# Performance work log

Measured on AMD Instinct MI355X. Metric: run time of the kernel, lower is better.

The kernel has to match this reference:

```python
import jax, jax.numpy as jnp
import numpy as np

EMBED_DIM = 1024
NUM_HEADS = 16
HEAD_DIM = EMBED_DIM // NUM_HEADS  # 64
SCALE = HEAD_DIM ** -0.5


def _rope_table(seq_len, dtype=jnp.float32):
    # inv_freq: [head_dim/2]
    inv_freq = 1.0 / (10000.0 ** (jnp.arange(0, HEAD_DIM, 2, dtype=dtype) / HEAD_DIM))
    t = jnp.arange(seq_len, dtype=dtype)
    freqs = t[:, None] * inv_freq[None, :]  # [S, hd/2]
    return jnp.sin(freqs), jnp.cos(freqs)


def _apply_rope(x, sin, cos):
    # x: [B, H, S, hd]; sin/cos: [S, hd/2]
    sin = sin[None, None]
    cos = cos[None, None]
    x_even = x[..., 0::2]
    x_odd = x[..., 1::2]
    new_even = x_even * cos - x_odd * sin
    new_odd = x_even * sin + x_odd * cos
    # interleave back: [..., hd/2, 2] -> [..., hd]
    return jnp.stack((new_even, new_odd), axis=-1).reshape(x.shape)


def setup_inputs() -> dict:
    key = jax.random.key(0)
    ks = jax.random.split(key, 9)
    B, S, D = 2, 2048, EMBED_DIM
    s = D ** -0.5
    return {
        "query": jax.random.normal(ks[0], (B, S, D), dtype=jnp.float32),
        "Wq": jax.random.normal(ks[1], (2 * D, D), dtype=jnp.float32) * s,
        "bq": jnp.zeros((2 * D,), dtype=jnp.float32),
        "Wk": jax.random.normal(ks[2], (D, D), dtype=jnp.float32) * s,
        "bk": jnp.zeros((D,), dtype=jnp.float32),
        "Wv": jax.random.normal(ks[3], (D, D), dtype=jnp.float32) * s,
        "bv": jnp.zeros((D,), dtype=jnp.float32),
        "Wo": jax.random.normal(ks[4], (D, D), dtype=jnp.float32) * s,
        "bo": jnp.zeros((D,), dtype=jnp.float32),
    }


def reference(query, Wq, bq, Wk, bk, Wv, bv, Wo, bo):
    B, S, D = query.shape
    H, hd = NUM_HEADS, HEAD_DIM

    # QKV projections (elementwise-gate variant: q_proj outputs 2*D)
    q_raw = (query @ Wq.T + bq).reshape(B, S, H, 2 * hd)
    q = q_raw[..., :hd].transpose(0, 2, 1, 3)          # [B,H,S,hd]
    gate = q_raw[..., hd:].transpose(0, 2, 1, 3)        # [B,H,S,hd]
    k = (query @ Wk.T + bk).reshape(B, S, H, hd).transpose(0, 2, 1, 3)
    v = (query @ Wv.T + bv).reshape(B, S, H, hd).transpose(0, 2, 1, 3)

    sin, cos = _rope_table(S)
    q = _apply_rope(q, sin, cos)
    k = _apply_rope(k, sin, cos)

    # scaled dot-product attention (no mask, non-causal, dropout=0)
    scores = jnp.einsum('bhqd,bhkd->bhqk', q, k) * SCALE
    probs = jax.nn.softmax(scores, axis=-1)
    attn = jnp.einsum('bhqk,bhkd->bhqd', probs, v)

    # sigmoid elementwise gate, then output projection
    attn = attn * jax.nn.sigmoid(gate)
    out = attn.transpose(0, 2, 1, 3).reshape(B, S, D)
    return out @ Wo.T + bo
```

## Files before the change

kernel.cpp:

```cpp
#include <hip/hip_runtime.h>
#include <math.h>

#define SEQ 2048
#define DIMD 1024
#define NH 16
#define HDIM 64

typedef _Float16 h8 __attribute__((ext_vector_type(8)));
typedef _Float16 h4 __attribute__((ext_vector_type(4)));
typedef __fp16 fp16x2 __attribute__((ext_vector_type(2)));
typedef float f32x4 __attribute__((ext_vector_type(4)));

typedef const __attribute__((address_space(1))) void* gas_t;
typedef __attribute__((address_space(3))) void* las_t;

__device__ __forceinline__ int SWE(int r, int c) {
  return ((r << 6) + c) ^ ((r & 7) << 3);
}

#define R0 16384
#define R1 (R0 + 1048576)
#define R2 (R1 + 524288)
#define R3 (R2 + 262144)
#define R4 (R3 + 262144)
#define R5 (R4 + 262144)

__global__ void prep_kernel(const float* __restrict__ query,
                            const float* __restrict__ Wq,
                            const float* __restrict__ Wk,
                            const float* __restrict__ Wv,
                            const float* __restrict__ Wo,
                            _Float16* __restrict__ Ah,
                            _Float16* __restrict__ Wqh,
                            _Float16* __restrict__ Wkh,
                            _Float16* __restrict__ Wvh,
                            _Float16* __restrict__ Woh,
                            float* __restrict__ sintab,
                            float* __restrict__ costab) {
  int i = blockIdx.x * 256 + threadIdx.x;
  if (i < R0) {
#pragma unroll
    for (int j = 0; j < 4; ++j) {
      int idx = i * 4 + j;
      int tp = idx >> 5;
      int fi = idx & 31;
      double inv = pow(10000.0, -(double)(2 * fi) / 64.0);
      double a = (double)tp * inv;
      sintab[idx] = (float)sin(a);
      costab[idx] = (float)cos(a);
    }
    return;
  }
  const float* src;
  _Float16* dst;
  int k;
  if (i < R1) {
    k = i - R0; src = query; dst = Ah;
  } else if (i < R2) {
    k = i - R1; src = Wq; dst = Wqh;
  } else if (i < R3) {
    k = i - R2; src = Wk; dst = Wkh;
  } else if (i < R4) {
    k = i - R3; src = Wv; dst = Wvh;
  } else if (i < R5) {
    k = i - R4; src = Wo; dst = Woh;
  } else {
    return;
  }
  float4 v = ((const float4*)src)[k];
  h4 H;
  H[0] = (_Float16)v.x;
  H[1] = (_Float16)v.y;
  H[2] = (_Float16)v.z;
  H[3] = (_Float16)v.w;
  ((h4*)dst)[k] = H;
}

__global__ __launch_bounds__(256) void qkv_kernel(
    const _Float16* __restrict__ Ah, const _Float16* __restrict__ Wqh,
    const _Float16* __restrict__ Wkh, const _Float16* __restrict__ Wvh,
    const float* __restrict__ bq, const float* __restrict__ bk,
    const float* __restrict__ bv, _Float16* __restrict__ qw,
    _Float16* __restrict__ sg, _Float16* __restrict__ kw,
    _Float16* __restrict__ vtw, const float* __restrict__ sintab,
    const float* __restrict__ costab) {
  __shared__ _Float16 Abuf[8192];
  __shared__ _Float16 Bbuf[8192];
  const int t = threadIdx.x;
  const int lane = t & 63;
  const int w = t >> 6;
  const int wm = w & 1, wn = w >> 1;
  const int fr = lane & 15;
  const int g = lane >> 4;
  const int m0 = blockIdx.y * 128;
  const int n0 = blockIdx.x * 128;
  const int region = (n0 < 2048) ? 0 : (n0 < 3072 ? 1 : 2);
  const _Float16* Wb = region == 0   ? Wqh + (size_t)n0 * DIMD
                       : region == 1 ? Wkh + (size_t)(n0 - 2048) * DIMD
                                     : Wvh + (size_t)(n0 - 3072) * DIMD;
  const float* bias = region == 0   ? bq + n0
                      : region == 1 ? bk + (n0 - 2048)
                                    : bv + (n0 - 3072);

  f32x4 acc[4][4];
#pragma unroll
  for (int i = 0; i < 4; ++i)
#pragma unroll
    for (int j = 0; j < 4; ++j) acc[i][j] = (f32x4){0.f, 0.f, 0.f, 0.f};

  const int rsub = t >> 3;
  const int csw = ((t & 7) ^ (rsub & 7)) << 3;
  const _Float16* gA = Ah + (size_t)(m0 + rsub) * DIMD + csw;
  const _Float16* gB = Wb + (size_t)rsub * DIMD + csw;
  const int dbase = (t >> 6) * 512 + 0;

  for (int kt = 0; kt < 16; ++kt) {
#pragma unroll
    for (int i = 0; i < 4; ++i) {
      __builtin_amdgcn_global_load_lds(
          (gas_t)(gA + (size_t)i * 32 * DIMD + kt * 64),
          (las_t)&Abuf[i * 2048 + w * 512], 16, 0, 0);
      __builtin_amdgcn_global_load_lds(
          (gas_t)(gB + (size_t)i * 32 * DIMD + kt * 64),
          (las_t)&Bbuf[i * 2048 + w * 512], 16, 0, 0);
    }
    __syncthreads();
#pragma unroll
    for (int s = 0; s < 2; ++s) {
      h8 av[4], bv[4];
#pragma unroll
      for (int mi = 0; mi < 4; ++mi)
        av[mi] = *(const h8*)&Abuf[SWE(wm * 64 + mi * 16 + fr, 8 * g + 32 * s)];
#pragma unroll
      for (int ni = 0; ni < 4; ++ni)
        bv[ni] = *(const h8*)&Bbuf[SWE(wn * 64 + ni * 16 + fr, 8 * g + 32 * s)];
      __builtin_amdgcn_s_setprio(1);
#pragma unroll
      for (int mi = 0; mi < 4; ++mi)
#pragma unroll
        for (int ni = 0; ni < 4; ++ni)
          acc[mi][ni] = __builtin_amdgcn_mfma_f32_16x16x32_f16(
              av[mi], bv[ni], acc[mi][ni], 0, 0, 0);
      __builtin_amdgcn_s_setprio(0);
    }
    __syncthreads();
  }

#pragma unroll
  for (int mi = 0; mi < 4; ++mi)
#pragma unroll
    for (int ni = 0; ni < 4; ++ni) {
      const int cl = wn * 64 + ni * 16 + fr;
      const float bsv = bias[cl];
      if (region == 2) {
        const int vc = (n0 - 3072) + cl;
        const int h = vc >> 6, d = vc & 63;
        const int row0 = m0 + wm * 64 + mi * 16 + g * 4;
        const int b = row0 >> 11;
        const int s0 = row0 & (SEQ - 1);
        h4 vv;
#pragma unroll
        for (int r = 0; r < 4; ++r) vv[r] = (_Float16)(acc[mi][ni][r] + bsv);
        *(h4*)&vtw[((size_t)(b * NH + h) * HDIM + d) * SEQ + s0] = vv;
        continue;
      }
#pragma unroll
      for (int r = 0; r < 4; ++r) {
        const int row = m0 + wm * 64 + mi * 16 + g * 4 + r;
        float v = acc[mi][ni][r] + bsv;
        const int b = row >> 11;
        const int s = row & (SEQ - 1);
        if (region == 0) {
          const int h = n0 >> 7;
          const int d = cl & 63;
          if (wn == 0) {
            float vp = __shfl_xor(v, 1);
            const int pi = s * 32 + (d >> 1);
            float sn = sintab[pi], cs = costab[pi];
            float rv = (d & 1) ? (vp * sn + v * cs) : (v * cs - vp * sn);
            rv *= 0.125f;
            qw[((size_t)(b * NH + h) * SEQ + s) * HDIM + d] = (_Float16)rv;
          } else {
            float gv = 1.0f / (1.0f + __expf(-v));
            sg[((size_t)(b * SEQ + s)) * DIMD + h * HDIM + d] = (_Float16)gv;
          }
        } else {
          const int kc = (n0 - 2048) + cl;
          const int h = kc >> 6, d = kc & 63;
          float vp = __shfl_xor(v, 1);
          const int pi = s * 32 + (d >> 1);
          float sn = sintab[pi], cs = costab[pi];
          float rv = (d & 1) ? (vp * sn + v * cs) : (v * cs - vp * sn);
          kw[((size_t)(b * NH + h) * SEQ + s) * HDIM + d] = (_Float16)rv;
        }
      }
    }
}

__global__ __launch_bounds__(256) void ogemm_kernel(
    const _Float16* __restrict__ ag, const _Float16* __restrict__ Woh,
    const float* __restrict__ bias, float* __restrict__ out) {
  __shared__ _Float16 Abuf[8192];
  __shared__ _Float16 Bbuf[4096];
  const int t = threadIdx.x;
  const int lane = t & 63;
  const int w = t >> 6;
  const int wm = w & 1, wn = w >> 1;
  const int fr = lane & 15;
  const int g = lane >> 4;
  const int m0 = blockIdx.y * 128, n0 = blockIdx.x * 64;

  f32x4 acc[4][2];
#pragma unroll
  for (int i = 0; i < 4; ++i)
#pragma unroll
    for (int j = 0; j < 2; ++j) acc[i][j] = (f32x4){0.f, 0.f, 0.f, 0.f};

  const int rsub = t >> 3;
  const int csw = ((t & 7) ^ (rsub & 7)) << 3;
  const _Float16* gA = ag + (size_t)(m0 + rsub) * DIMD + csw;
  const _Float16* gB = Woh + (size_t)(n0 + rsub) * DIMD + csw;

  for (int kt = 0; kt < 16; ++kt) {
#pragma unroll
    for (int i = 0; i < 4; ++i)
      __builtin_amdgcn_global_load_lds(
          (gas_t)(gA + (size_t)i * 32 * DIMD + kt * 64),
          (las_t)&Abuf[i * 2048 + w * 512], 16, 0, 0);
#pragma unroll
    for (int i = 0; i < 2; ++i)
      __builtin_amdgcn_global_load_lds(
          (gas_t)(gB + (size_t)i * 32 * DIMD + kt * 64),
          (las_t)&Bbuf[i * 2048 + w * 512], 16, 0, 0);
    __syncthreads();
#pragma unroll
    for (int s = 0; s < 2; ++s) {
      h8 av[4], bv[2];
#pragma unroll
      for (int mi = 0; mi < 4; ++mi)
        av[mi] = *(const h8*)&Abuf[SWE(wm * 64 + mi * 16 + fr, 8 * g + 32 * s)];
#pragma unroll
      for (int ni = 0; ni < 2; ++ni)
        bv[ni] = *(const h8*)&Bbuf[SWE(wn * 32 + ni * 16 + fr, 8 * g + 32 * s)];
      __builtin_amdgcn_s_setprio(1);
#pragma unroll
      for (int mi = 0; mi < 4; ++mi)
#pragma unroll
        for (int ni = 0; ni < 2; ++ni)
          acc[mi][ni] = __builtin_amdgcn_mfma_f32_16x16x32_f16(
              av[mi], bv[ni], acc[mi][ni], 0, 0, 0);
      __builtin_amdgcn_s_setprio(0);
    }
    __syncthreads();
  }

#pragma unroll
  for (int mi = 0; mi < 4; ++mi)
#pragma unroll
    for (int ni = 0; ni < 2; ++ni) {
      const int col = n0 + wn * 32 + ni * 16 + fr;
      const float bsv = bias[col];
#pragma unroll
      for (int r = 0; r < 4; ++r) {
        const int row = m0 + wm * 64 + mi * 16 + g * 4 + r;
        out[(size_t)row * DIMD + col] = acc[mi][ni][r] + bsv;
      }
    }
}

__global__ __launch_bounds__(256) void flash_kernel(
    const _Float16* __restrict__ qh, const _Float16* __restrict__ kh,
    const _Float16* __restrict__ vt, const _Float16* __restrict__ sg,
    _Float16* __restrict__ ag) {
  __shared__ _Float16 K_lds[4096];
  __shared__ _Float16 Vt_lds[4096];
  const int t = threadIdx.x;
  const int lane = t & 63;
  const int w = t >> 6;
  const int fr = lane & 15;
  const int g = lane >> 4;
  const int flat = blockIdx.x;
  const int swz = (flat & 7) * 128 + (flat >> 3);
  const int bh = swz >> 5;
  const int q0 = (swz & 31) * 64;
  const size_t kvbase = (size_t)bh * (SEQ * HDIM);

  h8 qb[2];
  {
    const _Float16* qp = qh + kvbase + (size_t)(q0 + 16 * w + fr) * HDIM + 8 * g;
    qb[0] = *(const h8*)(qp);
    qb[1] = *(const h8*)(qp + 32);
  }

  f32x4 oacc[4];
  float m_i = -1e30f, l_i = 0.f;
#pragma unroll
  for (int df = 0; df < 4; ++df) oacc[df] = (f32x4){0.f, 0.f, 0.f, 0.f};

  const int srow = t >> 2;
  const int scb = (t & 3) * 16;
  const _Float16* kp = kh + kvbase;
  const _Float16* vp = vt + kvbase + (size_t)srow * SEQ;

  h8 k0v = *(const h8*)(kp + (size_t)srow * HDIM + scb);
  h8 k1v = *(const h8*)(kp + (size_t)srow * HDIM + scb + 8);
  h8 v0v = *(const h8*)(vp + scb);
  h8 v1v = *(const h8*)(vp + scb + 8);

  for (int j0 = 0; j0 < SEQ; j0 += 64) {
    __syncthreads();
    *(h8*)&K_lds[SWE(srow, scb)] = k0v;
    *(h8*)&K_lds[SWE(srow, scb + 8)] = k1v;
    *(h8*)&Vt_lds[SWE(srow, scb)] = v0v;
    *(h8*)&Vt_lds[SWE(srow, scb + 8)] = v1v;
    if (j0 + 64 < SEQ) {
      k0v = *(const h8*)(kp + (size_t)(j0 + 64 + srow) * HDIM + scb);
      k1v = *(const h8*)(kp + (size_t)(j0 + 64 + srow) * HDIM + scb + 8);
      v0v = *(const h8*)(vp + j0 + 64 + scb);
      v1v = *(const h8*)(vp + j0 + 64 + scb + 8);
    }
    __syncthreads();

    f32x4 sacc[4];
#pragma unroll
    for (int nf = 0; nf < 4; ++nf) sacc[nf] = (f32x4){0.f, 0.f, 0.f, 0.f};

    __builtin_amdgcn_s_setprio(1);
#pragma unroll
    for (int nf = 0; nf < 4; ++nf) {
      h8 ka0 = *(const h8*)&K_lds[SWE(16 * nf + fr, 8 * g)];
      h8 ka1 = *(const h8*)&K_lds[SWE(16 * nf + fr, 32 + 8 * g)];
      sacc[nf] =
          __builtin_amdgcn_mfma_f32_16x16x32_f16(ka0, qb[0], sacc[nf], 0, 0, 0);
      sacc[nf] =
          __builtin_amdgcn_mfma_f32_16x16x32_f16(ka1, qb[1], sacc[nf], 0, 0, 0);
    }
    __builtin_amdgcn_s_setprio(0);

    float m0 = fmaxf(fmaxf(sacc[0][0], sacc[0][1]), sacc[0][2]);
    float m1 = fmaxf(fmaxf(sacc[0][3], sacc[1][0]), sacc[1][1]);
    float m2 = fmaxf(fmaxf(sacc[1][2], sacc[1][3]), sacc[2][0]);
    float m3 = fmaxf(fmaxf(sacc[2][1], sacc[2][2]), sacc[2][3]);
    float m4 = fmaxf(fmaxf(sacc[3][0], sacc[3][1]), sacc[3][2]);
    float mx =
        fmaxf(fmaxf(fmaxf(fmaxf(m0, m1), m2), fmaxf(m3, m4)), sacc[3][3]);
    mx = fmaxf(mx, __shfl_xor(mx, 16));
    mx = fmaxf(mx, __shfl_xor(mx, 32));
    const int allskip = __all(mx <= m_i + 8.0f);
    const float mn = allskip ? m_i : fmaxf(m_i, mx);
    float p[4][4];
    float rs = 0.f;
#pragma unroll
    for (int nf = 0; nf < 4; ++nf)
#pragma unroll
      for (int r = 0; r < 4; ++r) {
        p[nf][r] = __expf(sacc[nf][r] - mn);
        rs += p[nf][r];
      }
    rs += __shfl_xor(rs, 16);
    rs += __shfl_xor(rs, 32);
    if (allskip) {
      l_i += rs;
    } else {
      float f = __expf(m_i - mn);
      l_i = l_i * f + rs;
      m_i = mn;
      f32x4 fv = (f32x4){f, f, f, f};
#pragma unroll
      for (int df = 0; df < 4; ++df) oacc[df] *= fv;
    }
    h8 pb[2];
#pragma unroll
    for (int m2i = 0; m2i < 2; ++m2i) {
      union {
        h8 v;
        fp16x2 h[4];
      } u;
      u.h[0] = __builtin_amdgcn_cvt_pkrtz(p[2 * m2i][0], p[2 * m2i][1]);
      u.h[1] = __builtin_amdgcn_cvt_pkrtz(p[2 * m2i][2], p[2 * m2i][3]);
      u.h[2] = __builtin_amdgcn_cvt_pkrtz(p[2 * m2i + 1][0], p[2 * m2i + 1][1]);
      u.h[3] = __builtin_amdgcn_cvt_pkrtz(p[2 * m2i + 1][2], p[2 * m2i + 1][3]);
      pb[m2i] = u.v;
    }

    __builtin_amdgcn_s_setprio(1);
#pragma unroll
    for (int df = 0; df < 4; ++df) {
#pragma unroll
      for (int m2i = 0; m2i < 2; ++m2i) {
        h4 vlo = *(const h4*)&Vt_lds[SWE(16 * df + fr, 32 * m2i + 4 * g)];
        h4 vhi = *(const h4*)&Vt_lds[SWE(16 * df + fr, 32 * m2i + 16 + 4 * g)];
        h8 va;
#pragma unroll
        for (int r = 0; r < 4; ++r) {
          va[r] = vlo[r];
          va[4 + r] = vhi[r];
        }
        oacc[df] =
            __builtin_amdgcn_mfma_f32_16x16x32_f16(va, pb[m2i], oacc[df], 0, 0, 0);
      }
    }
    __builtin_amdgcn_s_setprio(0);
  }

  const int b = bh >> 4, h = bh & 15;
  const int qrow = q0 + 16 * w + fr;
  const float inv = 1.0f / l_i;
  const size_t obase = ((size_t)(b * SEQ + qrow)) * DIMD + h * HDIM;
#pragma unroll
  for (int df = 0; df < 4; ++df) {
    const int d0 = 16 * df + 4 * g;
    h4 gt = *(const h4*)&sg[obase + d0];
    h4 ov;
#pragma unroll
    for (int r = 0; r < 4; ++r)
      ov[r] = (_Float16)(oacc[df][r] * inv * (float)gt[r]);
    *(h4*)&ag[obase + d0] = ov;
  }
}

extern "C" void kernel_launch(void* const* d_in, const int* in_sizes, int n_in,
                              void* d_out, int out_size, void* d_ws,
                              size_t ws_size, hipStream_t stream) {
  const float* query = (const float*)d_in[0];
  const float* Wq = (const float*)d_in[1];
  const float* bq = (const float*)d_in[2];
  const float* Wk = (const float*)d_in[3];
  const float* bk = (const float*)d_in[4];
  const float* Wv = (const float*)d_in[5];
  const float* bv = (const float*)d_in[6];
  const float* Wo = (const float*)d_in[7];
  const float* bo = (const float*)d_in[8];
  float* out = (float*)d_out;

  float* fws = (float*)d_ws;
  float* sintab = fws;
  float* costab = fws + 65536;
  _Float16* Ah = (_Float16*)(fws + 131072);
  _Float16* Wqh = Ah + 4194304;
  _Float16* Wkh = Wqh + 2097152;
  _Float16* Wvh = Wkh + 1048576;
  _Float16* Woh = Wvh + 1048576;
  _Float16* qw = Woh + 1048576;
  _Float16* kw = qw + 4194304;
  _Float16* vtw = kw + 4194304;
  _Float16* sg = vtw + 4194304;
  _Float16* ag = Ah;

  prep_kernel<<<9280, 256, 0, stream>>>(query, Wq, Wk, Wv, Wo, Ah, Wqh, Wkh,
                                        Wvh, Woh, sintab, costab);

  qkv_kernel<<<dim3(32, 32), 256, 0, stream>>>(Ah, Wqh, Wkh, Wvh, bq, bk, bv,
                                               qw, sg, kw, vtw, sintab, costab);

  flash_kernel<<<1024, 256, 0, stream>>>(qw, kw, vtw, sg, ag);

  ogemm_kernel<<<dim3(16, 32), 256, 0, stream>>>(ag, Woh, bo, out);
}
```

Baseline: 161.6 us.

## Triple-buffer QKV GEMM with 256-row tiles and repack V in LDS

```diff
diff --git a/kernel.cpp b/kernel.cpp
--- a/kernel.cpp
+++ b/kernel.cpp
@@ -76,7 +76,7 @@
   ((h4*)dst)[k] = H;
 }
 
-__global__ __launch_bounds__(256) void qkv_kernel(
+__global__ __launch_bounds__(512) void qkv_kernel(
     const _Float16* __restrict__ Ah, const _Float16* __restrict__ Wqh,
     const _Float16* __restrict__ Wkh, const _Float16* __restrict__ Wvh,
     const float* __restrict__ bq, const float* __restrict__ bk,
@@ -84,15 +84,16 @@
     _Float16* __restrict__ sg, _Float16* __restrict__ kw,
     _Float16* __restrict__ vtw, const float* __restrict__ sintab,
     const float* __restrict__ costab) {
-  __shared__ _Float16 Abuf[8192];
-  __shared__ _Float16 Bbuf[8192];
+  __shared__ _Float16 Abuf[3][16384];
+  __shared__ _Float16 Bbuf[3][8192];
   const int t = threadIdx.x;
   const int lane = t & 63;
   const int w = t >> 6;
-  const int wm = w & 1, wn = w >> 1;
+  const int wm = w >> 1;
+  const int wn = w & 1;
   const int fr = lane & 15;
   const int g = lane >> 4;
-  const int m0 = blockIdx.y * 128;
+  const int m0 = blockIdx.y * 256;
   const int n0 = blockIdx.x * 128;
   const int region = (n0 < 2048) ? 0 : (n0 < 3072 ? 1 : 2);
   const _Float16* Wb = region == 0   ? Wqh + (size_t)n0 * DIMD
@@ -112,28 +113,44 @@
   const int csw = ((t & 7) ^ (rsub & 7)) << 3;
   const _Float16* gA = Ah + (size_t)(m0 + rsub) * DIMD + csw;
   const _Float16* gB = Wb + (size_t)rsub * DIMD + csw;
-  const int dbase = (t >> 6) * 512 + 0;
-
+
+  auto stage = [&](int kt, int bi) {
+#pragma unroll
+    for (int i = 0; i < 4; ++i)
+      __builtin_amdgcn_global_load_lds(
+          (gas_t)(gA + (size_t)i * 64 * DIMD + kt * 64),
+          (las_t)&Abuf[bi][i * 4096 + t * 8], 16, 0, 0);
+#pragma unroll
+    for (int i = 0; i < 2; ++i)
+      __builtin_amdgcn_global_load_lds(
+          (gas_t)(gB + (size_t)i * 64 * DIMD + kt * 64),
+          (las_t)&Bbuf[bi][i * 4096 + t * 8], 16, 0, 0);
+  };
+
+  stage(0, 0);
+  stage(1, 1);
   for (int kt = 0; kt < 16; ++kt) {
-#pragma unroll
-    for (int i = 0; i < 4; ++i) {
-      __builtin_amdgcn_global_load_lds(
-          (gas_t)(gA + (size_t)i * 32 * DIMD + kt * 64),
-          (las_t)&Abuf[i * 2048 + w * 512], 16, 0, 0);
-      __builtin_amdgcn_global_load_lds(
-          (gas_t)(gB + (size_t)i * 32 * DIMD + kt * 64),
-          (las_t)&Bbuf[i * 2048 + w * 512], 16, 0, 0);
-    }
-    __syncthreads();
-#pragma unroll
-    for (int s = 0; s < 2; ++s) {
+    const int cb = kt % 3;
+    if (kt + 1 < 16) {
+      asm volatile("s_waitcnt vmcnt(6)" ::: "memory");
+    } else {
+      asm volatile("s_waitcnt vmcnt(0)" ::: "memory");
+    }
+    if (kt + 2 < 16) stage(kt + 2, (kt + 2) % 3);
+    __builtin_amdgcn_sched_barrier(0);
+    __builtin_amdgcn_s_barrier();
+    __builtin_amdgcn_sched_barrier(0);
+#pragma unroll
+    for (int kk = 0; kk < 2; ++kk) {
       h8 av[4], bv[4];
 #pragma unroll
       for (int mi = 0; mi < 4; ++mi)
-        av[mi] = *(const h8*)&Abuf[SWE(wm * 64 + mi * 16 + fr, 8 * g + 32 * s)];
+        av[mi] =
+            *(const h8*)&Abuf[cb][SWE(wm * 64 + mi * 16 + fr, 8 * g + 32 * kk)];
 #pragma unroll
       for (int ni = 0; ni < 4; ++ni)
-        bv[ni] = *(const h8*)&Bbuf[SWE(wn * 64 + ni * 16 + fr, 8 * g + 32 * s)];
+        bv[ni] =
+            *(const h8*)&Bbuf[cb][SWE(wn * 64 + ni * 16 + fr, 8 * g + 32 * kk)];
       __builtin_amdgcn_s_setprio(1);
 #pragma unroll
       for (int mi = 0; mi < 4; ++mi)
@@ -143,7 +160,7 @@
               av[mi], bv[ni], acc[mi][ni], 0, 0, 0);
       __builtin_amdgcn_s_setprio(0);
     }
-    __syncthreads();
+    __builtin_amdgcn_s_barrier();
   }
 
 #pragma unroll
@@ -226,12 +243,12 @@
     for (int i = 0; i < 4; ++i)
       __builtin_amdgcn_global_load_lds(
           (gas_t)(gA + (size_t)i * 32 * DIMD + kt * 64),
-          (las_t)&Abuf[i * 2048 + w * 512], 16, 0, 0);
+          (las_t)&Abuf[i * 2048 + t * 8], 16, 0, 0);
 #pragma unroll
     for (int i = 0; i < 2; ++i)
       __builtin_amdgcn_global_load_lds(
           (gas_t)(gB + (size_t)i * 32 * DIMD + kt * 64),
-          (las_t)&Bbuf[i * 2048 + w * 512], 16, 0, 0);
+          (las_t)&Bbuf[i * 2048 + t * 8], 16, 0, 0);
     __syncthreads();
 #pragma unroll
     for (int s = 0; s < 2; ++s) {
@@ -299,6 +316,7 @@
 
   const int srow = t >> 2;
   const int scb = (t & 3) * 16;
+  const int vbase = ((scb >> 4) >> 1) * 32 + ((scb >> 4) & 1) * 4;
   const _Float16* kp = kh + kvbase;
   const _Float16* vp = vt + kvbase + (size_t)srow * SEQ;
 
@@ -311,8 +329,16 @@
     __syncthreads();
     *(h8*)&K_lds[SWE(srow, scb)] = k0v;
     *(h8*)&K_lds[SWE(srow, scb + 8)] = k1v;
-    *(h8*)&Vt_lds[SWE(srow, scb)] = v0v;
-    *(h8*)&Vt_lds[SWE(srow, scb + 8)] = v1v;
+    {
+      h4 a0 = __builtin_shufflevector(v0v, v0v, 0, 1, 2, 3);
+      h4 a1 = __builtin_shufflevector(v0v, v0v, 4, 5, 6, 7);
+      h4 b0 = __builtin_shufflevector(v1v, v1v, 0, 1, 2, 3);
+      h4 b1 = __builtin_shufflevector(v1v, v1v, 4, 5, 6, 7);
+      *(h4*)&Vt_lds[SWE(srow, vbase)] = a0;
+      *(h4*)&Vt_lds[SWE(srow, vbase + 8)] = a1;
+      *(h4*)&Vt_lds[SWE(srow, vbase + 16)] = b0;
+      *(h4*)&Vt_lds[SWE(srow, vbase + 24)] = b1;
+    }
     if (j0 + 64 < SEQ) {
       k0v = *(const h8*)(kp + (size_t)(j0 + 64 + srow) * HDIM + scb);
       k1v = *(const h8*)(kp + (size_t)(j0 + 64 + srow) * HDIM + scb + 8);
@@ -388,14 +414,7 @@
     for (int df = 0; df < 4; ++df) {
 #pragma unroll
       for (int m2i = 0; m2i < 2; ++m2i) {
-        h4 vlo = *(const h4*)&Vt_lds[SWE(16 * df + fr, 32 * m2i + 4 * g)];
-        h4 vhi = *(const h4*)&Vt_lds[SWE(16 * df + fr, 32 * m2i + 16 + 4 * g)];
-        h8 va;
-#pragma unroll
-        for (int r = 0; r < 4; ++r) {
-          va[r] = vlo[r];
-          va[4 + r] = vhi[r];
-        }
+        h8 va = *(const h8*)&Vt_lds[SWE(16 * df + fr, m2i * 32 + 8 * g)];
         oacc[df] =
             __builtin_amdgcn_mfma_f32_16x16x32_f16(va, pb[m2i], oacc[df], 0, 0, 0);
       }
@@ -450,7 +469,7 @@
   prep_kernel<<<9280, 256, 0, stream>>>(query, Wq, Wk, Wv, Wo, Ah, Wqh, Wkh,
                                         Wvh, Woh, sintab, costab);
 
-  qkv_kernel<<<dim3(32, 32), 256, 0, stream>>>(Ah, Wqh, Wkh, Wvh, bq, bk, bv,
+  qkv_kernel<<<dim3(32, 16), 512, 0, stream>>>(Ah, Wqh, Wkh, Wvh, bq, bk, bv,
                                                qw, sg, kw, vtw, sintab, costab);
 
   flash_kernel<<<1024, 256, 0, stream>>>(qw, kw, vtw, sg, ag);
```

Result: slower. 164.8 us (+2.0%).

## Stagger GEMM k-loop start per block and pre-permute V tile in LDS

Applied to the files above, without the earlier changes.

```diff
diff --git a/kernel.cpp b/kernel.cpp
--- a/kernel.cpp
+++ b/kernel.cpp
@@ -94,6 +94,7 @@
   const int g = lane >> 4;
   const int m0 = blockIdx.y * 128;
   const int n0 = blockIdx.x * 128;
+  const int phase = (blockIdx.x * 5 + blockIdx.y * 11) & 15;
   const int region = (n0 < 2048) ? 0 : (n0 < 3072 ? 1 : 2);
   const _Float16* Wb = region == 0   ? Wqh + (size_t)n0 * DIMD
                        : region == 1 ? Wkh + (size_t)(n0 - 2048) * DIMD
@@ -112,9 +113,9 @@
   const int csw = ((t & 7) ^ (rsub & 7)) << 3;
   const _Float16* gA = Ah + (size_t)(m0 + rsub) * DIMD + csw;
   const _Float16* gB = Wb + (size_t)rsub * DIMD + csw;
-  const int dbase = (t >> 6) * 512 + 0;
-
-  for (int kt = 0; kt < 16; ++kt) {
+
+  for (int it = 0; it < 16; ++it) {
+    const int kt = (it + phase) & 15;
 #pragma unroll
     for (int i = 0; i < 4; ++i) {
       __builtin_amdgcn_global_load_lds(
@@ -209,6 +210,7 @@
   const int fr = lane & 15;
   const int g = lane >> 4;
   const int m0 = blockIdx.y * 128, n0 = blockIdx.x * 64;
+  const int phase = (blockIdx.x * 5 + blockIdx.y * 11) & 15;
 
   f32x4 acc[4][2];
 #pragma unroll
@@ -221,17 +223,18 @@
   const _Float16* gA = ag + (size_t)(m0 + rsub) * DIMD + csw;
   const _Float16* gB = Woh + (size_t)(n0 + rsub) * DIMD + csw;
 
-  for (int kt = 0; kt < 16; ++kt) {
+  for (int it = 0; it < 16; ++it) {
+    const int kt = (it + phase) & 15;
 #pragma unroll
     for (int i = 0; i < 4; ++i)
       __builtin_amdgcn_global_load_lds(
           (gas_t)(gA + (size_t)i * 32 * DIMD + kt * 64),
-          (las_t)&Abuf[i * 2048 + w * 512], 16, 0, 0);
+          (las_t)&Abuf[i * 2048 + t * 8], 16, 0, 0);
 #pragma unroll
     for (int i = 0; i < 2; ++i)
       __builtin_amdgcn_global_load_lds(
           (gas_t)(gB + (size_t)i * 32 * DIMD + kt * 64),
-          (las_t)&Bbuf[i * 2048 + w * 512], 16, 0, 0);
+          (las_t)&Bbuf[i * 2048 + t * 8], 16, 0, 0);
     __syncthreads();
 #pragma unroll
     for (int s = 0; s < 2; ++s) {
@@ -299,6 +302,7 @@
 
   const int srow = t >> 2;
   const int scb = (t & 3) * 16;
+  const int vbase = ((scb >> 4) >> 1) * 32 + ((scb >> 4) & 1) * 4;
   const _Float16* kp = kh + kvbase;
   const _Float16* vp = vt + kvbase + (size_t)srow * SEQ;
 
@@ -311,8 +315,16 @@
     __syncthreads();
     *(h8*)&K_lds[SWE(srow, scb)] = k0v;
     *(h8*)&K_lds[SWE(srow, scb + 8)] = k1v;
-    *(h8*)&Vt_lds[SWE(srow, scb)] = v0v;
-    *(h8*)&Vt_lds[SWE(srow, scb + 8)] = v1v;
+    {
+      h4 a0 = __builtin_shufflevector(v0v, v0v, 0, 1, 2, 3);
+      h4 a1 = __builtin_shufflevector(v0v, v0v, 4, 5, 6, 7);
+      h4 b0 = __builtin_shufflevector(v1v, v1v, 0, 1, 2, 3);
+      h4 b1 = __builtin_shufflevector(v1v, v1v, 4, 5, 6, 7);
+      *(h4*)&Vt_lds[SWE(srow, vbase)] = a0;
+      *(h4*)&Vt_lds[SWE(srow, vbase + 8)] = a1;
+      *(h4*)&Vt_lds[SWE(srow, vbase + 16)] = b0;
+      *(h4*)&Vt_lds[SWE(srow, vbase + 24)] = b1;
+    }
     if (j0 + 64 < SEQ) {
       k0v = *(const h8*)(kp + (size_t)(j0 + 64 + srow) * HDIM + scb);
       k1v = *(const h8*)(kp + (size_t)(j0 + 64 + srow) * HDIM + scb + 8);
@@ -388,14 +400,7 @@
     for (int df = 0; df < 4; ++df) {
 #pragma unroll
       for (int m2i = 0; m2i < 2; ++m2i) {
-        h4 vlo = *(const h4*)&Vt_lds[SWE(16 * df + fr, 32 * m2i + 4 * g)];
-        h4 vhi = *(const h4*)&Vt_lds[SWE(16 * df + fr, 32 * m2i + 16 + 4 * g)];
-        h8 va;
-#pragma unroll
-        for (int r = 0; r < 4; ++r) {
-          va[r] = vlo[r];
-          va[4 + r] = vhi[r];
-        }
+        h8 va = *(const h8*)&Vt_lds[SWE(16 * df + fr, m2i * 32 + 8 * g)];
         oacc[df] =
             __builtin_amdgcn_mfma_f32_16x16x32_f16(va, pb[m2i], oacc[df], 0, 0, 0);
       }
```

Measured after the change: 168.0 us. +4.0%, slower.
